# Kernel optimization log

Measured on AMD Instinct MI355X. Metric: run time of the kernel, lower is better.

The kernel has to match this reference:

```python
import jax, jax.numpy as jnp
import numpy as np

VOCAB = 40000
EMB = 128
INNER = 128
Q_LEN = 20


def setup_inputs() -> dict:
    key = jax.random.key(0)
    ks = jax.random.split(key, 16)
    B, S, NB = 32, 512, 20
    std = 0.1
    inp = {
        "memories": jax.random.normal(ks[0], (B, S, NB, EMB), jnp.float32),
        "stories": jax.random.normal(ks[1], (B, S, EMB), jnp.float32),
        "stories_mask": jnp.ones((B, S), jnp.float32),
        "queries": jax.random.randint(ks[2], (B, Q_LEN), 0, VOCAB, jnp.int32),
        "keys": jax.random.randint(ks[3], (NB,), 0, VOCAB, jnp.int32),
        # learned parameters
        "emb_table": jax.random.normal(ks[4], (VOCAB, EMB), jnp.float32) * std,
        "mult_mask": jnp.ones((Q_LEN, EMB), jnp.float32),
        "A": jax.random.normal(ks[5], (EMB, INNER), jnp.float32) * std,
        "Bm": jax.random.normal(ks[6], (EMB, INNER), jnp.float32) * std,
        "C": jax.random.normal(ks[7], (EMB, INNER), jnp.float32) * std,
        "v": jnp.ones((INNER,), jnp.float32),
        "D": jax.random.normal(ks[8], (EMB, INNER), jnp.float32) * std,
        "E": jax.random.normal(ks[9], (EMB, INNER), jnp.float32) * std,
        "F": jax.random.normal(ks[10], (EMB, INNER), jnp.float32) * std,
        "w": jnp.ones((INNER,), jnp.float32),
        "H": jax.random.normal(ks[11], (EMB, EMB), jnp.float32) * std,
        "R": jax.random.normal(ks[12], (EMB, VOCAB), jnp.float32) * std,
    }
    return inp


def reference(memories, stories, stories_mask, queries, keys,
              emb_table, mult_mask, A, Bm, C, v, D, E, F, w, H, R):
    # _reduce_query: embed tokens, apply positional multiplicative mask, sum over positions
    u = jnp.sum(emb_table[queries] * mult_mask, axis=1)            # [B, emb]

    # intratemporal (Bahdanau-style) attention over memory blocks
    ia = jnp.einsum('bsne,ei->bsni', memories, A)                  # [B,S,NB,inner]
    kb = emb_table[keys] @ Bm                                      # [NB,inner]
    qc = u @ C                                                     # [B,inner]
    intr_align = jnp.sum(v * jnp.tanh(ia + kb[None, None] + qc[:, None, None]), axis=3)  # [B,S,NB]
    intr_attn = jax.nn.softmax(intr_align, axis=2)[..., None]      # [B,S,NB,1]
    temporal_memory = jnp.sum(intr_attn * memories, axis=2)        # [B,S,emb]

    # temporal attention over story sentences (with sentence term E, softmax activation)
    td = temporal_memory @ D                                       # [B,S,inner]
    te = stories @ E                                               # [B,S,inner]
    tf = (u @ F)[:, None]                                          # [B,1,inner]
    temporal_align_unmasked = jnp.sum(w * jnp.tanh(td + te + tf), axis=2)  # [B,S]
    temporal_align = temporal_align_unmasked * stories_mask
    # softmax branch: additive -inf mask where stories_mask == 0 (inf*0 NaNs zeroed in torch)
    masked_logits = jnp.where(stories_mask != 0, temporal_align, -jnp.inf)
    temporal_attn = jax.nn.softmax(masked_logits, axis=1)          # [B,S]

    # output readout (standard memory-network head)
    o = jnp.sum(temporal_attn[..., None] * temporal_memory, axis=1)  # [B,emb]
    logits = (o + u @ H) @ R                                         # [B,vocab]
    return logits
```

## Files before the change

kernel.cpp:

```cpp
#include <hip/hip_runtime.h>
#include <hip/hip_bf16.h>

#define B_   32
#define S_   512
#define NB_  20
#define EMB_ 128
#define VOC_ 40000

typedef float f32x4 __attribute__((ext_vector_type(4)));
typedef _Float16 f16x8 __attribute__((ext_vector_type(8)));
typedef __fp16 fp16x2 __attribute__((ext_vector_type(2)));

union FragH { uint4 u; f16x8 h; };
union H2 { fp16x2 h; unsigned u; };

__device__ __forceinline__ unsigned pk2(float a, float b){
  H2 t; t.h = __builtin_amdgcn_cvt_pkrtz(a, b);
  return t.u;
}
__device__ __forceinline__ unsigned short f2h(float x){
  _Float16 h = (_Float16)x;
  return __builtin_bit_cast(unsigned short, h);
}
__device__ __forceinline__ float tanh_fast(float x){
  float xx = fminf(fmaxf(x, -15.f), 15.f);
  float e = __expf(2.f*xx);
  return (e-1.f)/(e+1.f);
}


__global__ __launch_bounds__(128) void prep_kernel(
    const int* __restrict__ queries, const int* __restrict__ keys,
    const float* __restrict__ emb, const float* __restrict__ mmask,
    const float* __restrict__ A, const float* __restrict__ Bm,
    const float* __restrict__ C, const float* __restrict__ D,
    const float* __restrict__ E, const float* __restrict__ F,
    const float* __restrict__ H,
    float* __restrict__ qc_w, float* __restrict__ tf_w,
    float* __restrict__ uh_w, float* __restrict__ kb_w,
    unsigned short* __restrict__ afrag, unsigned short* __restrict__ w2frag)
{
  int bid = blockIdx.x, tid = threadIdx.x;
  if (bid < 32) {
    __shared__ float ulds[128];
    int b = bid;
    float s = 0.f;
    for (int q=0;q<NB_;q++){
      int tok = queries[b*NB_+q];
      s += emb[tok*128+tid]*mmask[q*128+tid];
    }
    ulds[tid] = s;
    __syncthreads();
    float sq=0.f, sf=0.f, sh=0.f;
    for (int e=0;e<128;e++){
      float uv = ulds[e];
      sq += uv*C[e*128+tid];
      sf += uv*F[e*128+tid];
      sh += uv*H[e*128+tid];
    }
    qc_w[b*128+tid]=sq; tf_w[b*128+tid]=sf; uh_w[b*128+tid]=sh;
  } else if (bid < 52) {
    __shared__ float ek[128];
    int n = bid-32;
    int tok = keys[n];
    ek[tid] = emb[tok*128+tid];
    __syncthreads();
    float s=0.f;
    for (int e=0;e<128;e++) s += ek[e]*Bm[e*128+tid];
    kb_w[n*128+tid] = s;
  } else if (bid < 60) {
    int a = bid-52;
    for (int cc=0;cc<2;cc++){
      int c = (a*128+tid)*2+cc;
      int lane = c&63, kc = (c>>6)&3, nt = c>>8;
      int n2 = nt*16 + (lane&15);
      int k0 = kc*32 + (lane>>4)*8;
      alignas(16) unsigned short t[8];
      #pragma unroll
      for (int j=0;j<8;j++) t[j] = f2h(A[(k0+j)*128+n2]);
      *(uint4*)(afrag + c*8) = *(const uint4*)t;
    }
  } else {
    int wb = bid-60;
    for (int cc=0;cc<2;cc++){
      int c = (wb*128+tid)*2+cc;
      int lane = c&63, kc = (c>>6)&7, nt = c>>9;
      int n2 = nt*16 + (lane&15);
      int k0 = kc*32 + (lane>>4)*8;
      alignas(16) unsigned short t[8];
      #pragma unroll
      for (int j=0;j<8;j++){
        int k = k0+j;
        float x = (k<128) ? D[k*128+n2] : E[(k-128)*128+n2];
        t[j] = f2h(x);
      }
      *(uint4*)(w2frag + c*8) = *(const uint4*)t;
    }
  }
}

__global__ __launch_bounds__(256) void k2a_kernel(
    const float* __restrict__ mem, const unsigned short* __restrict__ afrag,
    const float* __restrict__ kb_w, const float* __restrict__ qc_w,
    const float* __restrict__ vvec, float* __restrict__ tm_w)
{
  __shared__ unsigned short mfr[5*4*64*8];
  __shared__ float alignP[4*80];
  __shared__ float aligns[80];
  __shared__ float attns[80];

  int g = blockIdx.x, tid = threadIdx.x;
  int b = g >> 7;

  const float4* gm = (const float4*)(mem) + (size_t)g*2560;
  #pragma unroll
  for (int it=0; it<10; ++it){
    int i4 = tid + it*256;
    float4 d = gm[i4];
    int e4 = i4*4;
    int row = e4 >> 7;
    int k = e4 & 127;
    int mt = row>>4, r = row&15;
    int kg = k>>5, s2 = (k>>3)&3;
    int slot = (s2<<4) | ((r ^ s2 ^ ((kg&1)<<2)) & 15);
    int chunk = (mt*4+kg)*64 + slot;
    *(uint2*)(mfr + chunk*8 + (k&7)) = make_uint2(pk2(d.x,d.y), pk2(d.z,d.w));
  }
  __syncthreads();

  int w = tid>>6, lane = tid&63;
  int lo16 = lane & 15, hi16 = lane >> 4;

  f32x4 acc[5][2];
  #pragma unroll
  for (int mt=0;mt<5;mt++){ acc[mt][0]=(f32x4)(0.f); acc[mt][1]=(f32x4)(0.f); }

  #pragma unroll
  for (int kc=0;kc<4;kc++){
    FragH b0, b1;
    b0.u = *(const uint4*)(afrag + ((size_t)((2*w)*4+kc)*64 + lane)*8);
    b1.u = *(const uint4*)(afrag + ((size_t)((2*w+1)*4+kc)*64 + lane)*8);
    int slot = (hi16<<4) | ((lo16 ^ hi16 ^ ((kc&1)<<2)) & 15);
    #pragma unroll
    for (int mt=0;mt<5;mt++){
      FragH a;
      a.u = *(const uint4*)(mfr + ((mt*4+kc)*64 + slot)*8);
      acc[mt][0] = __builtin_amdgcn_mfma_f32_16x16x32_f16(a.h, b0.h, acc[mt][0], 0,0,0);
      acc[mt][1] = __builtin_amdgcn_mfma_f32_16x16x32_f16(a.h, b1.h, acc[mt][1], 0,0,0);
    }
  }

  #pragma unroll
  for (int mt=0;mt<5;mt++){
    #pragma unroll
    for (int r=0;r<4;r++){
      unsigned row = mt*16 + hi16*4 + r;
      unsigned p = row/20u;
      unsigned n = row - p*20u;
      float part = 0.f;
      #pragma unroll
      for (int t2=0;t2<2;t2++){
        int col = (2*w+t2)*16 + lo16;
        float z = acc[mt][t2][r] + kb_w[n*128+col] + qc_w[b*128+col];
        part += vvec[col]*tanh_fast(z);
      }
      part += __shfl_xor(part, 1);
      part += __shfl_xor(part, 2);
      part += __shfl_xor(part, 4);
      part += __shfl_xor(part, 8);
      if (lo16 == 0) alignP[w*80+row] = part;
    }
  }
  __syncthreads();
  if (tid < 80){
    aligns[tid] = alignP[tid] + alignP[80+tid] + alignP[160+tid] + alignP[240+tid];
  }
  __syncthreads();
  if (tid < 4){
    float mx = -1e30f;
    for (int n=0;n<NB_;n++) mx = fmaxf(mx, aligns[tid*NB_+n]);
    float s = 0.f;
    for (int n=0;n<NB_;n++){ float e = __expf(aligns[tid*NB_+n]-mx); attns[tid*NB_+n]=e; s+=e; }
    float inv = 1.f/s;
    for (int n=0;n<NB_;n++) attns[tid*NB_+n] *= inv;
  }
  __syncthreads();

  {
    int p2 = tid>>6, e0 = (tid&63)*2;
    int kg = e0>>5, s2 = (e0>>3)&3;
    float2 o = make_float2(0.f,0.f);
    #pragma unroll
    for (int n=0;n<NB_;n++){
      int row = p2*NB_+n;
      float a = attns[row];
      int mt = row>>4, r = row&15;
      int slot = (s2<<4) | ((r ^ s2 ^ ((kg&1)<<2)) & 15);
      int chunk = (mt*4+kg)*64 + slot;
      H2 q; q.u = *(const unsigned*)(mfr + chunk*8 + (e0&7));
      o.x += a*(float)q.h[0];
      o.y += a*(float)q.h[1];
    }
    *(float2*)(tm_w + ((size_t)g*4+p2)*128 + e0) = o;
  }
}

__global__ __launch_bounds__(256) void k2b_kernel(
    const float* __restrict__ tm_w, const float* __restrict__ stories,
    const unsigned short* __restrict__ w2frag, const float* __restrict__ tf_w,
    const float* __restrict__ wvec, const float* __restrict__ smask,
    float* __restrict__ talign_w)
{
  __shared__ unsigned short afr[512*8];
  __shared__ float partial[4*16];
  int gb = blockIdx.x, tid = threadIdx.x;
  int flat0 = gb*16;
  int b = flat0 >> 9;

  #pragma unroll
  for (int it=0;it<2;it++){
    int c = tid + it*256;
    int lane = c&63, kc = c>>6;
    int p = lane&15;
    int k0 = kc*32 + (lane>>4)*8;
    const float* src = (k0 < 128)
        ? (tm_w + ((size_t)(flat0+p))*128 + k0)
        : (stories + ((size_t)(flat0+p))*128 + (k0-128));
    float4 s0 = *(const float4*)(src);
    float4 s1 = *(const float4*)(src+4);
    uint4 pkd;
    pkd.x = pk2(s0.x,s0.y); pkd.y = pk2(s0.z,s0.w);
    pkd.z = pk2(s1.x,s1.y); pkd.w = pk2(s1.z,s1.w);
    *(uint4*)(afr + c*8) = pkd;
  }
  __syncthreads();

  int w = tid>>6, lane = tid&63;
  int lo = lane&15, hi = lane>>4;
  f32x4 acc0 = (f32x4)(0.f), acc1 = (f32x4)(0.f);

  #pragma unroll
  for (int kc=0;kc<8;kc++){
    FragH af, b0, b1;
    af.u = *(const uint4*)(afr + (kc*64+lane)*8);
    b0.u = *(const uint4*)(w2frag + ((size_t)((2*w)*8+kc)*64+lane)*8);
    b1.u = *(const uint4*)(w2frag + ((size_t)((2*w+1)*8+kc)*64+lane)*8);
    acc0 = __builtin_amdgcn_mfma_f32_16x16x32_f16(af.h, b0.h, acc0, 0,0,0);
    acc1 = __builtin_amdgcn_mfma_f32_16x16x32_f16(af.h, b1.h, acc1, 0,0,0);
  }

  #pragma unroll
  for (int r=0;r<4;r++){
    int prow = hi*4+r;
    float part = 0.f;
    {
      int i0 = (2*w)*16+lo;
      part += wvec[i0]*tanh_fast(acc0[r] + tf_w[b*128+i0]);
      int i1 = (2*w+1)*16+lo;
      part += wvec[i1]*tanh_fast(acc1[r] + tf_w[b*128+i1]);
    }
    part += __shfl_xor(part,1);
    part += __shfl_xor(part,2);
    part += __shfl_xor(part,4);
    part += __shfl_xor(part,8);
    if (lo==0) partial[w*16+prow] = part;
  }
  __syncthreads();
  if (tid<16){
    float ta = partial[tid]+partial[16+tid]+partial[32+tid]+partial[48+tid];
    int flat = flat0+tid;
    float m = smask[flat];
    talign_w[flat] = (m != 0.0f) ? ta*m : -INFINITY;
  }
}

__global__ __launch_bounds__(256) void k3_kernel(
    const float* __restrict__ talign_w, const float* __restrict__ tm_w,
    const float* __restrict__ uh_w, float* __restrict__ ov_w)
{
  __shared__ float attn[512];
  __shared__ float red[256];
  int bid = blockIdx.x, tid = threadIdx.x;
  int b = bid >> 3, ec = bid & 7;

  float v0 = talign_w[b*512+tid];
  float v1 = talign_w[b*512+256+tid];
  red[tid] = fmaxf(v0,v1);
  __syncthreads();
  for (int s=128;s>0;s>>=1){ if (tid<s) red[tid]=fmaxf(red[tid],red[tid+s]); __syncthreads(); }
  float M = red[0];
  __syncthreads();
  float e0v = __expf(v0-M), e1v = __expf(v1-M);
  red[tid] = e0v+e1v;
  __syncthreads();
  for (int s=128;s>0;s>>=1){ if (tid<s) red[tid]+=red[tid+s]; __syncthreads(); }
  float invZ = 1.f/red[0];
  attn[tid] = e0v*invZ;
  attn[256+tid] = e1v*invZ;
  __syncthreads();

  int e = ec*16 + (tid&15);
  int sg = tid>>4;
  const float* tmb = tm_w + ((size_t)b*512 + sg*32)*128 + e;
  float a = 0.f;
  #pragma unroll 8
  for (int i=0;i<32;i++) a += attn[sg*32+i]*tmb[(size_t)i*128];
  red[tid] = a;
  __syncthreads();
  for (int s=128;s>=16;s>>=1){ if (tid<s) red[tid]+=red[tid+s]; __syncthreads(); }
  if (tid<16) ov_w[b*128+ec*16+tid] = red[tid]+uh_w[b*128+ec*16+tid];
}

__global__ __launch_bounds__(256) void k4_kernel(
    const float* __restrict__ ov_w, const float* __restrict__ R,
    float* __restrict__ out)
{
  int tid = threadIdx.x;
  int j = blockIdx.x*128 + (tid&63)*2;
  if (j >= VOC_) return;
  int bh = tid>>6;
  const float* ovb = ov_w + bh*8*128;
  float2 acc[8];
  #pragma unroll
  for (int bb=0;bb<8;bb++) acc[bb]=make_float2(0.f,0.f);
  for (int e=0;e<128;e+=4){
    float2 r0 = *(const float2*)(&R[(size_t)(e+0)*VOC_ + j]);
    float2 r1 = *(const float2*)(&R[(size_t)(e+1)*VOC_ + j]);
    float2 r2 = *(const float2*)(&R[(size_t)(e+2)*VOC_ + j]);
    float2 r3 = *(const float2*)(&R[(size_t)(e+3)*VOC_ + j]);
    #pragma unroll
    for (int bb=0;bb<8;bb++){
      float4 o = *(const float4*)(&ovb[bb*128+e]);
      acc[bb].x += o.x*r0.x + o.y*r1.x + o.z*r2.x + o.w*r3.x;
      acc[bb].y += o.x*r0.y + o.y*r1.y + o.z*r2.y + o.w*r3.y;
    }
  }
  #pragma unroll
  for (int bb=0;bb<8;bb++)
    *(float2*)(&out[(size_t)(bh*8+bb)*VOC_ + j]) = acc[bb];
}

extern "C" void kernel_launch(void* const* d_in, const int* in_sizes, int n_in,
                              void* d_out, int out_size, void* d_ws, size_t ws_size,
                              hipStream_t stream)
{
  const float* mem    = (const float*)d_in[0];
  const float* stories= (const float*)d_in[1];
  const float* smask  = (const float*)d_in[2];
  const int*   queries= (const int*)d_in[3];
  const int*   keys   = (const int*)d_in[4];
  const float* emb    = (const float*)d_in[5];
  const float* mmask  = (const float*)d_in[6];
  const float* A      = (const float*)d_in[7];
  const float* Bm     = (const float*)d_in[8];
  const float* C      = (const float*)d_in[9];
  const float* vvec   = (const float*)d_in[10];
  const float* D      = (const float*)d_in[11];
  const float* E      = (const float*)d_in[12];
  const float* F      = (const float*)d_in[13];
  const float* wvec   = (const float*)d_in[14];
  const float* H      = (const float*)d_in[15];
  const float* R      = (const float*)d_in[16];
  float* out = (float*)d_out;

  char* ws = (char*)d_ws;
  float* qc_w             = (float*)(ws + 0);
  float* tf_w             = (float*)(ws + 16384);
  float* uh_w             = (float*)(ws + 32768);
  float* kb_w             = (float*)(ws + 49152);
  unsigned short* afrag   = (unsigned short*)(ws + 60416);
  unsigned short* w2frag  = (unsigned short*)(ws + 93184);
  float* tm_w             = (float*)(ws + 158720);
  float* talign_w         = (float*)(ws + 8547328);
  float* ov_w             = (float*)(ws + 8612864);

  prep_kernel<<<76,128,0,stream>>>(queries, keys, emb, mmask, A, Bm, C, D, E, F, H,
                                   qc_w, tf_w, uh_w, kb_w, afrag, w2frag);
  k2a_kernel<<<4096,256,0,stream>>>(mem, afrag, kb_w, qc_w, vvec, tm_w);
  k2b_kernel<<<1024,256,0,stream>>>(tm_w, stories, w2frag, tf_w, wvec, smask, talign_w);
  k3_kernel<<<256,256,0,stream>>>(talign_w, tm_w, uh_w, ov_w);
  k4_kernel<<<313,256,0,stream>>>(ov_w, R, out);
}
```

Baseline: 368.2 us.

## Fuse temporal-alignment GEMM into intratemporal kernel and store temporal memory as fp16

Merges the second-stage kernel, which computes the story alignment from temporal memory and stories, into the intratemporal attention kernel. Each block now builds its 4-row MFMA A-fragment straight from LDS instead of re-reading temporal memory from global. Temporal memory is written in fp16, which halves the workspace traffic read later by the readout kernel, and that kernel now accumulates over packed half pairs. The cost is extra LDS syncs and MFMA tiles that are only 25% used, since only 4 of 16 rows are valid, plus some extra rounding error from fp16.

```diff
diff --git a/kernel.cpp b/kernel.cpp
--- a/kernel.cpp
+++ b/kernel.cpp
@@ -99,18 +99,26 @@
   }
 }
 
-__global__ __launch_bounds__(256) void k2a_kernel(
+__global__ __launch_bounds__(256) void k2_kernel(
     const float* __restrict__ mem, const unsigned short* __restrict__ afrag,
     const float* __restrict__ kb_w, const float* __restrict__ qc_w,
-    const float* __restrict__ vvec, float* __restrict__ tm_w)
+    const float* __restrict__ vvec,
+    const float* __restrict__ stories, const unsigned short* __restrict__ w2frag,
+    const float* __restrict__ tf_w, const float* __restrict__ wvec,
+    const float* __restrict__ smask,
+    unsigned short* __restrict__ tm_h, float* __restrict__ talign_w)
 {
   __shared__ unsigned short mfr[5*4*64*8];
   __shared__ float alignP[4*80];
   __shared__ float aligns[80];
   __shared__ float attns[80];
+  __shared__ float partial2[16];
 
   int g = blockIdx.x, tid = threadIdx.x;
   int b = g >> 7;
+
+  int p2 = tid>>6, e0 = (tid&63)*2;
+  float2 sto = *(const float2*)(stories + ((size_t)(g*4+p2))*128 + e0);
 
   const float4* gm = (const float4*)(mem) + (size_t)g*2560;
   #pragma unroll
@@ -131,44 +139,46 @@
   int w = tid>>6, lane = tid&63;
   int lo16 = lane & 15, hi16 = lane >> 4;
 
-  f32x4 acc[5][2];
-  #pragma unroll
-  for (int mt=0;mt<5;mt++){ acc[mt][0]=(f32x4)(0.f); acc[mt][1]=(f32x4)(0.f); }
-
-  #pragma unroll
-  for (int kc=0;kc<4;kc++){
-    FragH b0, b1;
-    b0.u = *(const uint4*)(afrag + ((size_t)((2*w)*4+kc)*64 + lane)*8);
-    b1.u = *(const uint4*)(afrag + ((size_t)((2*w+1)*4+kc)*64 + lane)*8);
-    int slot = (hi16<<4) | ((lo16 ^ hi16 ^ ((kc&1)<<2)) & 15);
+  {
+    f32x4 acc[5][2];
+    #pragma unroll
+    for (int mt=0;mt<5;mt++){ acc[mt][0]=(f32x4)(0.f); acc[mt][1]=(f32x4)(0.f); }
+
+    #pragma unroll
+    for (int kc=0;kc<4;kc++){
+      FragH b0, b1;
+      b0.u = *(const uint4*)(afrag + ((size_t)((2*w)*4+kc)*64 + lane)*8);
+      b1.u = *(const uint4*)(afrag + ((size_t)((2*w+1)*4+kc)*64 + lane)*8);
+      int slot = (hi16<<4) | ((lo16 ^ hi16 ^ ((kc&1)<<2)) & 15);
+      #pragma unroll
+      for (int mt=0;mt<5;mt++){
+        FragH a;
+        a.u = *(const uint4*)(mfr + ((mt*4+kc)*64 + slot)*8);
+        acc[mt][0] = __builtin_amdgcn_mfma_f32_16x16x32_f16(a.h, b0.h, acc[mt][0], 0,0,0);
+        acc[mt][1] = __builtin_amdgcn_mfma_f32_16x16x32_f16(a.h, b1.h, acc[mt][1], 0,0,0);
+      }
+    }
+
     #pragma unroll
     for (int mt=0;mt<5;mt++){
-      FragH a;
-      a.u = *(const uint4*)(mfr + ((mt*4+kc)*64 + slot)*8);
-      acc[mt][0] = __builtin_amdgcn_mfma_f32_16x16x32_f16(a.h, b0.h, acc[mt][0], 0,0,0);
-      acc[mt][1] = __builtin_amdgcn_mfma_f32_16x16x32_f16(a.h, b1.h, acc[mt][1], 0,0,0);
-    }
-  }
-
-  #pragma unroll
-  for (int mt=0;mt<5;mt++){
-    #pragma unroll
-    for (int r=0;r<4;r++){
-      unsigned row = mt*16 + hi16*4 + r;
-      unsigned p = row/20u;
-      unsigned n = row - p*20u;
-      float part = 0.f;
-      #pragma unroll
-      for (int t2=0;t2<2;t2++){
-        int col = (2*w+t2)*16 + lo16;
-        float z = acc[mt][t2][r] + kb_w[n*128+col] + qc_w[b*128+col];
-        part += vvec[col]*tanh_fast(z);
+      #pragma unroll
+      for (int r=0;r<4;r++){
+        unsigned row = mt*16 + hi16*4 + r;
+        unsigned p = row/20u;
+        unsigned n = row - p*20u;
+        float part = 0.f;
+        #pragma unroll
+        for (int t2=0;t2<2;t2++){
+          int col = (2*w+t2)*16 + lo16;
+          float z = acc[mt][t2][r] + kb_w[n*128+col] + qc_w[b*128+col];
+          part += vvec[col]*tanh_fast(z);
+        }
+        part += __shfl_xor(part, 1);
+        part += __shfl_xor(part, 2);
+        part += __shfl_xor(part, 4);
+        part += __shfl_xor(part, 8);
+        if (lo16 == 0) alignP[w*80+row] = part;
       }
-      part += __shfl_xor(part, 1);
-      part += __shfl_xor(part, 2);
-      part += __shfl_xor(part, 4);
-      part += __shfl_xor(part, 8);
-      if (lo16 == 0) alignP[w*80+row] = part;
     }
   }
   __syncthreads();
@@ -186,8 +196,8 @@
   }
   __syncthreads();
 
+  unsigned otm;
   {
-    int p2 = tid>>6, e0 = (tid&63)*2;
     int kg = e0>>5, s2 = (e0>>3)&3;
     float2 o = make_float2(0.f,0.f);
     #pragma unroll
@@ -201,85 +211,61 @@
       o.x += a*(float)q.h[0];
       o.y += a*(float)q.h[1];
     }
-    *(float2*)(tm_w + ((size_t)g*4+p2)*128 + e0) = o;
-  }
-}
-
-__global__ __launch_bounds__(256) void k2b_kernel(
-    const float* __restrict__ tm_w, const float* __restrict__ stories,
-    const unsigned short* __restrict__ w2frag, const float* __restrict__ tf_w,
-    const float* __restrict__ wvec, const float* __restrict__ smask,
-    float* __restrict__ talign_w)
-{
-  __shared__ unsigned short afr[512*8];
-  __shared__ float partial[4*16];
-  int gb = blockIdx.x, tid = threadIdx.x;
-  int flat0 = gb*16;
-  int b = flat0 >> 9;
-
-  #pragma unroll
-  for (int it=0;it<2;it++){
-    int c = tid + it*256;
-    int lane = c&63, kc = c>>6;
-    int p = lane&15;
-    int k0 = kc*32 + (lane>>4)*8;
-    const float* src = (k0 < 128)
-        ? (tm_w + ((size_t)(flat0+p))*128 + k0)
-        : (stories + ((size_t)(flat0+p))*128 + (k0-128));
-    float4 s0 = *(const float4*)(src);
-    float4 s1 = *(const float4*)(src+4);
-    uint4 pkd;
-    pkd.x = pk2(s0.x,s0.y); pkd.y = pk2(s0.z,s0.w);
-    pkd.z = pk2(s1.x,s1.y); pkd.w = pk2(s1.z,s1.w);
-    *(uint4*)(afr + c*8) = pkd;
-  }
-  __syncthreads();
-
-  int w = tid>>6, lane = tid&63;
-  int lo = lane&15, hi = lane>>4;
-  f32x4 acc0 = (f32x4)(0.f), acc1 = (f32x4)(0.f);
-
-  #pragma unroll
-  for (int kc=0;kc<8;kc++){
-    FragH af, b0, b1;
-    af.u = *(const uint4*)(afr + (kc*64+lane)*8);
-    b0.u = *(const uint4*)(w2frag + ((size_t)((2*w)*8+kc)*64+lane)*8);
-    b1.u = *(const uint4*)(w2frag + ((size_t)((2*w+1)*8+kc)*64+lane)*8);
-    acc0 = __builtin_amdgcn_mfma_f32_16x16x32_f16(af.h, b0.h, acc0, 0,0,0);
-    acc1 = __builtin_amdgcn_mfma_f32_16x16x32_f16(af.h, b1.h, acc1, 0,0,0);
-  }
-
-  #pragma unroll
-  for (int r=0;r<4;r++){
-    int prow = hi*4+r;
-    float part = 0.f;
-    {
-      int i0 = (2*w)*16+lo;
-      part += wvec[i0]*tanh_fast(acc0[r] + tf_w[b*128+i0]);
-      int i1 = (2*w+1)*16+lo;
-      part += wvec[i1]*tanh_fast(acc1[r] + tf_w[b*128+i1]);
-    }
-    part += __shfl_xor(part,1);
-    part += __shfl_xor(part,2);
-    part += __shfl_xor(part,4);
-    part += __shfl_xor(part,8);
-    if (lo==0) partial[w*16+prow] = part;
-  }
-  __syncthreads();
-  if (tid<16){
-    float ta = partial[tid]+partial[16+tid]+partial[32+tid]+partial[48+tid];
-    int flat = flat0+tid;
+    otm = pk2(o.x, o.y);
+    *(unsigned*)(tm_h + ((size_t)g*4+p2)*128 + e0) = otm;
+  }
+  __syncthreads();
+
+  {
+    int kc = e0>>5;
+    int lane2 = (((e0>>3)&3)<<4) | p2;
+    *(unsigned*)(mfr + (kc*64+lane2)*8 + (e0&7)) = otm;
+    *(unsigned*)(mfr + ((kc+4)*64+lane2)*8 + (e0&7)) = pk2(sto.x, sto.y);
+  }
+  __syncthreads();
+
+  {
+    f32x4 acc0 = (f32x4)(0.f), acc1 = (f32x4)(0.f);
+    #pragma unroll
+    for (int kc=0;kc<8;kc++){
+      FragH af, b0, b1;
+      af.u = *(const uint4*)(mfr + (kc*64+lane)*8);
+      b0.u = *(const uint4*)(w2frag + ((size_t)((2*w)*8+kc)*64+lane)*8);
+      b1.u = *(const uint4*)(w2frag + ((size_t)((2*w+1)*8+kc)*64+lane)*8);
+      acc0 = __builtin_amdgcn_mfma_f32_16x16x32_f16(af.h, b0.h, acc0, 0,0,0);
+      acc1 = __builtin_amdgcn_mfma_f32_16x16x32_f16(af.h, b1.h, acc1, 0,0,0);
+    }
+    if (hi16 == 0){
+      #pragma unroll
+      for (int r=0;r<4;r++){
+        int i0 = (2*w)*16+lo16;
+        float part = wvec[i0]*tanh_fast(acc0[r] + tf_w[b*128+i0]);
+        int i1 = (2*w+1)*16+lo16;
+        part += wvec[i1]*tanh_fast(acc1[r] + tf_w[b*128+i1]);
+        part += __shfl_xor(part,1);
+        part += __shfl_xor(part,2);
+        part += __shfl_xor(part,4);
+        part += __shfl_xor(part,8);
+        if (lo16==0) partial2[w*4+r] = part;
+      }
+    }
+  }
+  __syncthreads();
+  if (tid<4){
+    float ta = partial2[tid]+partial2[4+tid]+partial2[8+tid]+partial2[12+tid];
+    int flat = g*4+tid;
     float m = smask[flat];
     talign_w[flat] = (m != 0.0f) ? ta*m : -INFINITY;
   }
 }
 
 __global__ __launch_bounds__(256) void k3_kernel(
-    const float* __restrict__ talign_w, const float* __restrict__ tm_w,
+    const float* __restrict__ talign_w, const unsigned short* __restrict__ tm_h,
     const float* __restrict__ uh_w, float* __restrict__ ov_w)
 {
   __shared__ float attn[512];
   __shared__ float red[256];
+  __shared__ float2 red2[256];
   int bid = blockIdx.x, tid = threadIdx.x;
   int b = bid >> 3, ec = bid & 7;
 
@@ -299,16 +285,28 @@
   attn[256+tid] = e1v*invZ;
   __syncthreads();
 
-  int e = ec*16 + (tid&15);
-  int sg = tid>>4;
-  const float* tmb = tm_w + ((size_t)b*512 + sg*32)*128 + e;
-  float a = 0.f;
+  int e = ec*16 + (tid&7)*2;
+  int sg = tid>>3;
+  const unsigned short* tmb = tm_h + ((size_t)b*512 + sg*16)*128 + e;
+  float2 a2 = make_float2(0.f,0.f);
   #pragma unroll 8
-  for (int i=0;i<32;i++) a += attn[sg*32+i]*tmb[(size_t)i*128];
-  red[tid] = a;
-  __syncthreads();
-  for (int s=128;s>=16;s>>=1){ if (tid<s) red[tid]+=red[tid+s]; __syncthreads(); }
-  if (tid<16) ov_w[b*128+ec*16+tid] = red[tid]+uh_w[b*128+ec*16+tid];
+  for (int i=0;i<16;i++){
+    H2 q; q.u = *(const unsigned*)(tmb + (size_t)i*128);
+    float at = attn[sg*16+i];
+    a2.x += at*(float)q.h[0];
+    a2.y += at*(float)q.h[1];
+  }
+  red2[tid] = a2;
+  __syncthreads();
+  for (int s=128;s>=8;s>>=1){
+    if (tid<s){ red2[tid].x += red2[tid+s].x; red2[tid].y += red2[tid+s].y; }
+    __syncthreads();
+  }
+  if (tid<8){
+    int e2 = ec*16 + tid*2;
+    ov_w[b*128+e2]   = red2[tid].x + uh_w[b*128+e2];
+    ov_w[b*128+e2+1] = red2[tid].y + uh_w[b*128+e2+1];
+  }
 }
 
 __global__ __launch_bounds__(256) void k4_kernel(
@@ -370,14 +368,15 @@
   float* kb_w             = (float*)(ws + 49152);
   unsigned short* afrag   = (unsigned short*)(ws + 60416);
   unsigned short* w2frag  = (unsigned short*)(ws + 93184);
-  float* tm_w             = (float*)(ws + 158720);
-  float* talign_w         = (float*)(ws + 8547328);
-  float* ov_w             = (float*)(ws + 8612864);
+  unsigned short* tm_h    = (unsigned short*)(ws + 158720);
+  float* talign_w         = (float*)(ws + 4353024);
+  float* ov_w             = (float*)(ws + 4418560);
 
   prep_kernel<<<76,128,0,stream>>>(queries, keys, emb, mmask, A, Bm, C, D, E, F, H,
                                    qc_w, tf_w, uh_w, kb_w, afrag, w2frag);
-  k2a_kernel<<<4096,256,0,stream>>>(mem, afrag, kb_w, qc_w, vvec, tm_w);
-  k2b_kernel<<<1024,256,0,stream>>>(tm_w, stories, w2frag, tf_w, wvec, smask, talign_w);
-  k3_kernel<<<256,256,0,stream>>>(talign_w, tm_w, uh_w, ov_w);
+  k2_kernel<<<4096,256,0,stream>>>(mem, afrag, kb_w, qc_w, vvec,
+                                   stories, w2frag, tf_w, wvec, smask,
+                                   tm_h, talign_w);
+  k3_kernel<<<256,256,0,stream>>>(talign_w, tm_h, uh_w, ov_w);
   k4_kernel<<<313,256,0,stream>>>(ov_w, R, out);
 }
```

New measurement: 374.1 us. No clear change (+1.6%).
